# Kernel optimization log

Hardware: AMD Instinct MI355X
Metric: run time of the kernel (lower is better)

The kernel has to match this reference:

```python
import jax, jax.numpy as jnp
import numpy as np

B, T, D = 4, 2048, 1024

def setup_inputs() -> dict:
    key = jax.random.key(0)
    kx, kq, kk, kv = jax.random.split(key, 4)
    return {
        "vector": jax.random.normal(kx, (B, T, D), dtype=jnp.float32),
        # original uses torch.rand -> uniform [0,1)
        "W_queries": jax.random.uniform(kq, (D, D), dtype=jnp.float32),
        "W_keys": jax.random.uniform(kk, (D, D), dtype=jnp.float32),
        "W_values": jax.random.uniform(kv, (D, D), dtype=jnp.float32),
    }

def reference(vector, W_queries, W_keys, W_values):
    b, num_token, d_out = vector.shape
    queries = vector @ W_queries          # [b, t, d]
    keys = vector @ W_keys                # [b, t, d]
    values = vector @ W_values            # [b, t, d]
    # attention_score: [b, q, k]
    scores = jnp.einsum('bqd,bkd->bqk', queries, keys)
    causal_mask = jnp.triu(jnp.ones((num_token, num_token), dtype=bool), k=1)
    scores = jnp.where(causal_mask[None, :, :], -jnp.inf, scores)
    # NOTE: original uses FLOOR division `//` by sqrt(d_k) -- faithful here.
    inv_sqrt_scale = jnp.asarray(np.sqrt(keys.shape[-1]), dtype=scores.dtype)
    weights = jnp.floor(scores / inv_sqrt_scale)
    # NOTE: original applies softmax over dim=1 (the query axis), not dim=-1.
    weights = jax.nn.softmax(weights, axis=1)
    # dropout rate is 0.0 (eval/deterministic): identity
    context = jnp.einsum('bqk,bkd->bqd', weights, values)
    return context
```

## Files before the change

kernel.cpp:

```cpp
#include <hip/hip_runtime.h>
#include <math.h>

typedef _Float16 half4 __attribute__((ext_vector_type(4)));
typedef _Float16 half8 __attribute__((ext_vector_type(8)));
typedef float f32x4 __attribute__((ext_vector_type(4)));

#define GLD16(gptr, lptr)                                                     \
    __builtin_amdgcn_global_load_lds(                                         \
        (const __attribute__((address_space(1))) unsigned int*)(gptr),        \
        (__attribute__((address_space(3))) unsigned int*)(lptr), 16, 0, 0)

#define PIPE_SYNC()                                                           \
    do {                                                                      \
        asm volatile("s_waitcnt vmcnt(0)" ::: "memory");                      \
        __builtin_amdgcn_s_barrier();                                         \
    } while (0)

namespace {

constexpr int Bb = 4;
constexpr int Tt = 2048;
constexpr int Dd = 1024;
constexpr int BT = Bb * Tt;
constexpr int NCH = 16;

__device__ inline _Float16 f2h(float f) { return (_Float16)f; }

__global__ __launch_bounds__(256) void convert_x_kernel(
    const float* __restrict__ X, _Float16* __restrict__ Xhi, _Float16* __restrict__ Xlo)
{
    const int idx = (blockIdx.x * 256 + threadIdx.x) * 4;
    const float4 v = *(const float4*)(X + idx);
    const float a[4] = {v.x, v.y, v.z, v.w};
    half4 h, l;
#pragma unroll
    for (int i = 0; i < 4; ++i) {
        h[i] = f2h(a[i]);
        l[i] = f2h(a[i] - (float)h[i]);
    }
    *(half4*)(Xhi + idx) = h;
    *(half4*)(Xlo + idx) = l;
}

__global__ __launch_bounds__(256) void convert_wqk_kernel(
    const float* __restrict__ Wq, const float* __restrict__ Wk,
    _Float16* __restrict__ Wqh, _Float16* __restrict__ Wql,
    _Float16* __restrict__ Wkh, _Float16* __restrict__ Wkl)
{
    const int mat = blockIdx.y;
    const float* W = mat ? Wk : Wq;
    _Float16* Hh = mat ? Wkh : Wqh;
    _Float16* Ll = mat ? Wkl : Wql;
    const int idx = (blockIdx.x * 256 + threadIdx.x) * 4;
    const float4 v = *(const float4*)(W + idx);
    const float a[4] = {v.x, v.y, v.z, v.w};
    half4 h, l;
#pragma unroll
    for (int i = 0; i < 4; ++i) {
        h[i] = f2h(a[i]);
        l[i] = f2h(a[i] - (float)h[i]);
    }
    *(half4*)(Hh + idx) = h;
    *(half4*)(Ll + idx) = l;
}

__global__ __launch_bounds__(256) void convert_wv_kernel(
    const float* __restrict__ Wv, _Float16* __restrict__ WvTh)
{
    __shared__ float tile[64][65];
    const int n0 = blockIdx.x * 64, k0 = blockIdx.y * 64;
    const int tx = threadIdx.x & 63, ty = threadIdx.x >> 6;
#pragma unroll
    for (int i = 0; i < 16; ++i)
        tile[ty + i * 4][tx] = Wv[(size_t)(k0 + ty + i * 4) * Dd + n0 + tx];
    __syncthreads();
#pragma unroll
    for (int i = 0; i < 16; ++i) {
        const float v = tile[tx][ty + i * 4];
        WvTh[(size_t)(n0 + ty + i * 4) * Dd + k0 + tx] = f2h(v);
    }
}

__global__ __launch_bounds__(256) void gt_kernel(
    const _Float16* __restrict__ Wkh, const _Float16* __restrict__ Wkl,
    const _Float16* __restrict__ Wqh, const _Float16* __restrict__ Wql,
    _Float16* __restrict__ GTh, _Float16* __restrict__ GTl)
{
    __shared__ _Float16 Ahl[2][2][4][512];
    __shared__ _Float16 Bhl[2][2][4][512];

    const int n0 = blockIdx.x * 64;
    const int m0 = blockIdx.y * 64;
    const int tid = threadIdx.x;
    const int w = tid >> 6, lane = tid & 63;
    const int lr = lane & 15, lq = lane >> 4;
    const int wi = (w >> 1) * 2, wj = (w & 1) * 2;

    f32x4 acc[2][2];
#pragma unroll
    for (int i = 0; i < 2; ++i)
#pragma unroll
        for (int j = 0; j < 2; ++j)
#pragma unroll
            for (int c = 0; c < 4; ++c) acc[i][j][c] = 0.f;

    auto stage = [&](int bf, int kk) {
        const int s = w;
        const size_t ar = (size_t)(m0 + s * 16 + lr) * Dd + kk + lq * 8;
        const size_t br = (size_t)(n0 + s * 16 + lr) * Dd + kk + lq * 8;
        GLD16(Wkh + ar, &Ahl[bf][0][s][0]);
        GLD16(Wkl + ar, &Ahl[bf][1][s][0]);
        GLD16(Wqh + br, &Bhl[bf][0][s][0]);
        GLD16(Wql + br, &Bhl[bf][1][s][0]);
    };

    stage(0, 0);
    PIPE_SYNC();
    int ib = 0;
    for (int kk = 0; kk < 1024; kk += 32, ib ^= 1) {
        if (kk + 32 < 1024) stage(ib ^ 1, kk + 32);
        half8 ah[2], al[2], bh[2], bl[2];
#pragma unroll
        for (int i = 0; i < 2; ++i) {
            ah[i] = *(const half8*)&Ahl[ib][0][wi + i][lane * 8];
            al[i] = *(const half8*)&Ahl[ib][1][wi + i][lane * 8];
        }
#pragma unroll
        for (int j = 0; j < 2; ++j) {
            bh[j] = *(const half8*)&Bhl[ib][0][wj + j][lane * 8];
            bl[j] = *(const half8*)&Bhl[ib][1][wj + j][lane * 8];
        }
#pragma unroll
        for (int i = 0; i < 2; ++i)
#pragma unroll
            for (int j = 0; j < 2; ++j) {
                acc[i][j] = __builtin_amdgcn_mfma_f32_16x16x32_f16(ah[i], bh[j], acc[i][j], 0, 0, 0);
                acc[i][j] = __builtin_amdgcn_mfma_f32_16x16x32_f16(ah[i], bl[j], acc[i][j], 0, 0, 0);
                acc[i][j] = __builtin_amdgcn_mfma_f32_16x16x32_f16(al[i], bh[j], acc[i][j], 0, 0, 0);
            }
        PIPE_SYNC();
    }

#pragma unroll
    for (int i = 0; i < 2; ++i)
#pragma unroll
        for (int r = 0; r < 4; ++r) {
            const int row = m0 + (wi + i) * 16 + lq * 4 + r;
#pragma unroll
            for (int j = 0; j < 2; ++j) {
                const int col = n0 + (wj + j) * 16 + lr;
                const float v = acc[i][j][r];
                const _Float16 h = f2h(v);
                GTh[(size_t)row * Dd + col] = h;
                GTl[(size_t)row * Dd + col] = f2h(v - (float)h);
            }
        }
}

__global__ __launch_bounds__(256, 4) void tv_kernel(
    const _Float16* __restrict__ Xhi, const _Float16* __restrict__ Xlo,
    const _Float16* __restrict__ GTh, const _Float16* __restrict__ GTl,
    const _Float16* __restrict__ WvTh,
    _Float16* __restrict__ Thi, _Float16* __restrict__ Tlo,
    _Float16* __restrict__ Vrow)
{
    __shared__ _Float16 Ahl[2][8][512];
    __shared__ _Float16 Bhl[2][8][512];

    const int f  = blockIdx.x;
    const int fp = (f & 7) * 128 + (f >> 3);
    const int mb  = fp >> 4;
    const int sub = fp & 15;
    const int m0 = mb * 128;
    const int n0 = (sub & 7) * 128;

    const int tid = threadIdx.x;
    const int w = tid >> 6, lane = tid & 63;
    const int lr = lane & 15, lq = lane >> 4;
    const int wr = (w >> 1) * 4, wc = (w & 1) * 4;

    f32x4 acc[4][4];
#pragma unroll
    for (int i = 0; i < 4; ++i)
#pragma unroll
        for (int j = 0; j < 4; ++j)
#pragma unroll
            for (int c = 0; c < 4; ++c) acc[i][j][c] = 0.f;

    if (sub < 8) {
        for (int kk = 0; kk < 1024; kk += 32) {
            __syncthreads();
#pragma unroll
            for (int s2 = 0; s2 < 2; ++s2) {
                const int s = w * 2 + s2;
                const size_t ar = (size_t)(m0 + s * 16 + lr) * Dd + kk + lq * 8;
                const size_t br = (size_t)(n0 + s * 16 + lr) * Dd + kk + lq * 8;
                GLD16(Xhi + ar, &Ahl[0][s][0]);
                GLD16(Xlo + ar, &Ahl[1][s][0]);
                GLD16(GTh + br, &Bhl[0][s][0]);
                GLD16(GTl + br, &Bhl[1][s][0]);
            }
            __syncthreads();
            half8 ah[4], al[4], bh[4], bl[4];
#pragma unroll
            for (int i = 0; i < 4; ++i) {
                ah[i] = *(const half8*)&Ahl[0][wr + i][lane * 8];
                al[i] = *(const half8*)&Ahl[1][wr + i][lane * 8];
            }
#pragma unroll
            for (int j = 0; j < 4; ++j) {
                bh[j] = *(const half8*)&Bhl[0][wc + j][lane * 8];
                bl[j] = *(const half8*)&Bhl[1][wc + j][lane * 8];
            }
#pragma unroll
            for (int i = 0; i < 4; ++i)
#pragma unroll
                for (int j = 0; j < 4; ++j) {
                    acc[i][j] = __builtin_amdgcn_mfma_f32_16x16x32_f16(ah[i], bh[j], acc[i][j], 0, 0, 0);
                    acc[i][j] = __builtin_amdgcn_mfma_f32_16x16x32_f16(ah[i], bl[j], acc[i][j], 0, 0, 0);
                    acc[i][j] = __builtin_amdgcn_mfma_f32_16x16x32_f16(al[i], bh[j], acc[i][j], 0, 0, 0);
                }
        }
#pragma unroll
        for (int i = 0; i < 4; ++i)
#pragma unroll
            for (int r = 0; r < 4; ++r) {
                const int row = m0 + (wr + i) * 16 + lq * 4 + r;
#pragma unroll
                for (int j = 0; j < 4; ++j) {
                    const int col = n0 + (wc + j) * 16 + lr;
                    const float v = acc[i][j][r];
                    const _Float16 h = f2h(v);
                    Thi[(size_t)row * Dd + col] = h;
                    Tlo[(size_t)row * Dd + col] = f2h(v - (float)h);
                }
            }
    } else {
        for (int kk = 0; kk < 1024; kk += 32) {
            __syncthreads();
#pragma unroll
            for (int s2 = 0; s2 < 2; ++s2) {
                const int s = w * 2 + s2;
                GLD16(Xhi + (size_t)(m0 + s * 16 + lr) * Dd + kk + lq * 8, &Ahl[0][s][0]);
                GLD16(WvTh + (size_t)(n0 + s * 16 + lr) * Dd + kk + lq * 8, &Bhl[0][s][0]);
            }
            __syncthreads();
            half8 a[4], b2[4];
#pragma unroll
            for (int i = 0; i < 4; ++i) a[i] = *(const half8*)&Ahl[0][wr + i][lane * 8];
#pragma unroll
            for (int j = 0; j < 4; ++j) b2[j] = *(const half8*)&Bhl[0][wc + j][lane * 8];
#pragma unroll
            for (int i = 0; i < 4; ++i)
#pragma unroll
                for (int j = 0; j < 4; ++j)
                    acc[i][j] = __builtin_amdgcn_mfma_f32_16x16x32_f16(a[i], b2[j], acc[i][j], 0, 0, 0);
        }
#pragma unroll
        for (int i = 0; i < 4; ++i)
#pragma unroll
            for (int r = 0; r < 4; ++r) {
                const int row = m0 + (wr + i) * 16 + lq * 4 + r;
#pragma unroll
                for (int j = 0; j < 4; ++j)
                    Vrow[(size_t)row * Dd + n0 + (wc + j) * 16 + lr] = f2h(acc[i][j][r]);
            }
    }
}

__global__ __launch_bounds__(256) void transpose_v_kernel(
    const _Float16* __restrict__ Vrow, const float* __restrict__ Lb,
    _Float16* __restrict__ Vt)
{
    __shared__ _Float16 tile[64][78];
    const int d0 = blockIdx.x * 64, t0 = blockIdx.y * 64, b = blockIdx.z;
    const int tx = threadIdx.x & 63, ty = threadIdx.x >> 6;
#pragma unroll
    for (int i = 0; i < 16; ++i)
        tile[ty + i * 4][tx] = Vrow[((size_t)b * Tt + t0 + ty + i * 4) * Dd + d0 + tx];
    __syncthreads();
    const float sc = Lb[(size_t)b * Tt + t0 + tx];
#pragma unroll
    for (int i = 0; i < 16; ++i) {
        const float v = (float)tile[tx][ty + i * 4] * sc;
        Vt[(size_t)b * Dd * Tt + (size_t)(d0 + ty + i * 4) * Tt + t0 + tx] = f2h(v);
    }
}

__global__ __launch_bounds__(256) void scores_mfma_kernel(
    const _Float16* __restrict__ Thi, const _Float16* __restrict__ Tlo,
    const _Float16* __restrict__ Xhi, const _Float16* __restrict__ Xlo,
    float* __restrict__ S, float* __restrict__ Pm, float* __restrict__ Pl)
{
    const int f  = blockIdx.x;
    const int fp = (f & 7) * 68 + (f >> 3);
    const int b = fp / 136;
    const int t = fp - b * 136;
    int byi = (int)((sqrtf(8.f * t + 1.f) - 1.f) * 0.5f);
    if ((byi + 1) * (byi + 2) / 2 <= t) ++byi;
    if (byi * (byi + 1) / 2 > t) --byi;
    const int bxi = t - byi * (byi + 1) / 2;
    const int j0 = bxi * 128, q0 = byi * 128;
    float* Sb = S + (size_t)b * Tt * Tt;

    __shared__ _Float16 Ahl[2][2][8][512];
    __shared__ _Float16 Bhl[2][2][8][512];
    const _Float16* Th = Thi + (size_t)b * Tt * Dd;
    const _Float16* Tl = Tlo + (size_t)b * Tt * Dd;
    const _Float16* Xh = Xhi + (size_t)b * Tt * Dd;
    const _Float16* Xl = Xlo + (size_t)b * Tt * Dd;

    const int tid = threadIdx.x;
    const int w = tid >> 6, lane = tid & 63;
    const int lr = lane & 15, lq = lane >> 4;
    const int wr = (w >> 1) * 4, wc = (w & 1) * 4;

    f32x4 acc[4][4];
#pragma unroll
    for (int i = 0; i < 4; ++i)
#pragma unroll
        for (int j = 0; j < 4; ++j)
#pragma unroll
            for (int c = 0; c < 4; ++c) acc[i][j][c] = 0.f;

    auto stage = [&](int bf, int kk) {
#pragma unroll
        for (int s2 = 0; s2 < 2; ++s2) {
            const int s = w * 2 + s2;
            const size_t ar = (size_t)(q0 + s * 16 + lr) * Dd + kk + lq * 8;
            const size_t br = (size_t)(j0 + s * 16 + lr) * Dd + kk + lq * 8;
            GLD16(Th + ar, &Ahl[bf][0][s][0]);
            GLD16(Tl + ar, &Ahl[bf][1][s][0]);
            GLD16(Xh + br, &Bhl[bf][0][s][0]);
            GLD16(Xl + br, &Bhl[bf][1][s][0]);
        }
    };

    stage(0, 0);
    PIPE_SYNC();
    int ib = 0;
    for (int kk = 0; kk < 1024; kk += 32, ib ^= 1) {
        if (kk + 32 < 1024) stage(ib ^ 1, kk + 32);
        half8 ah[4], al[4], bh[4], bl[4];
#pragma unroll
        for (int i = 0; i < 4; ++i) {
            ah[i] = *(const half8*)&Ahl[ib][0][wr + i][lane * 8];
            al[i] = *(const half8*)&Ahl[ib][1][wr + i][lane * 8];
        }
#pragma unroll
        for (int j = 0; j < 4; ++j) {
            bh[j] = *(const half8*)&Bhl[ib][0][wc + j][lane * 8];
            bl[j] = *(const half8*)&Bhl[ib][1][wc + j][lane * 8];
        }
#pragma unroll
        for (int i = 0; i < 4; ++i)
#pragma unroll
            for (int j = 0; j < 4; ++j) {
                acc[i][j] = __builtin_amdgcn_mfma_f32_16x16x32_f16(ah[i], bh[j], acc[i][j], 0, 0, 0);
                acc[i][j] = __builtin_amdgcn_mfma_f32_16x16x32_f16(ah[i], bl[j], acc[i][j], 0, 0, 0);
                acc[i][j] = __builtin_amdgcn_mfma_f32_16x16x32_f16(al[i], bh[j], acc[i][j], 0, 0, 0);
            }
        PIPE_SYNC();
    }

    float sv[4][4][4];
#pragma unroll
    for (int i = 0; i < 4; ++i)
#pragma unroll
        for (int r = 0; r < 4; ++r) {
            const int q = q0 + (wr + i) * 16 + lq * 4 + r;
#pragma unroll
            for (int j = 0; j < 4; ++j) {
                const int jg = j0 + (wc + j) * 16 + lr;
                const float v = (jg <= q) ? floorf(acc[i][j][r] * 0.03125f) : -INFINITY;
                sv[i][j][r] = v;
                Sb[(size_t)q * Tt + jg] = v;
            }
        }

    float* red  = (float*)&Ahl[0][0][0][0];
    float* colm = red + 2048;
    __syncthreads();
    for (int e = tid; e < 2048; e += 256) red[e] = -INFINITY;
    __syncthreads();
    const int rowidx = (w * 4 + lq) * 128;
#pragma unroll
    for (int j = 0; j < 4; ++j) {
        const int c = (wc + j) * 16 + lr;
        float lm = -INFINITY;
#pragma unroll
        for (int i = 0; i < 4; ++i)
#pragma unroll
            for (int r = 0; r < 4; ++r) lm = fmaxf(lm, sv[i][j][r]);
        red[rowidx + c] = lm;
    }
    __syncthreads();
    if (tid < 128) {
        float m = -INFINITY;
#pragma unroll
        for (int e = 0; e < 16; ++e) m = fmaxf(m, red[e * 128 + tid]);
        colm[tid] = m;
    }
    __syncthreads();
    float ls[4];
#pragma unroll
    for (int j = 0; j < 4; ++j) {
        const int c = (wc + j) * 16 + lr;
        const float m = colm[c];
        float s = 0.f;
#pragma unroll
        for (int i = 0; i < 4; ++i)
#pragma unroll
            for (int r = 0; r < 4; ++r)
                if (sv[i][j][r] != -INFINITY) s += __expf(sv[i][j][r] - m);
        ls[j] = s;
    }
    __syncthreads();
    for (int e = tid; e < 2048; e += 256) red[e] = 0.f;
    __syncthreads();
#pragma unroll
    for (int j = 0; j < 4; ++j) red[rowidx + (wc + j) * 16 + lr] = ls[j];
    __syncthreads();
    if (tid < 128) {
        float l = 0.f;
#pragma unroll
        for (int e = 0; e < 16; ++e) l += red[e * 128 + tid];
        const size_t o = ((size_t)b * NCH + byi) * Tt + j0 + tid;
        Pm[o] = colm[tid];
        Pl[o] = l;
    }
}

__global__ __launch_bounds__(256) void colstats_merge_kernel(
    const float* __restrict__ Pm, const float* __restrict__ Pl,
    float* __restrict__ Mb, float* __restrict__ Lb)
{
    const int j = blockIdx.x * 256 + threadIdx.x;
    const int b = blockIdx.y;
    const int jt = j >> 7;
    float m = -INFINITY, l = 0.f;
    for (int c = jt; c < NCH; ++c) {
        const size_t pidx = ((size_t)b * NCH + c) * Tt + j;
        const float mi = Pm[pidx];
        if (mi == -INFINITY) continue;
        const float li = Pl[pidx];
        if (mi > m) { l = l * __expf(m - mi) + li; m = mi; }
        else        { l += li * __expf(mi - m); }
    }
    Mb[(size_t)b * Tt + j] = m;
    Lb[(size_t)b * Tt + j] = (l > 0.f) ? 1.f / l : 0.f;
}

__global__ __launch_bounds__(256) void pmat_kernel(
    const float* __restrict__ S, const float* __restrict__ Mb,
    _Float16* __restrict__ P)
{
    const int t = blockIdx.x;
    int byi = (int)((sqrtf(8.f * t + 1.f) - 1.f) * 0.5f);
    if ((byi + 1) * (byi + 2) / 2 <= t) ++byi;
    if (byi * (byi + 1) / 2 > t) --byi;
    const int bxi = t - byi * (byi + 1) / 2;
    const int b = blockIdx.z;
    const int j0 = bxi * 128, q0 = byi * 128;

    const int tr = threadIdx.x >> 4;
    const int tc = (threadIdx.x & 15) * 8;
    const float* mp = Mb + (size_t)b * Tt + j0 + tc;
    float mv[8];
#pragma unroll
    for (int e = 0; e < 8; ++e) mv[e] = mp[e];

#pragma unroll
    for (int it = 0; it < 8; ++it) {
        const int row = q0 + it * 16 + tr;
        const float* Sp = S + (size_t)b * Tt * Tt + (size_t)row * Tt + j0 + tc;
        const float4 s0 = *(const float4*)Sp;
        const float4 s1 = *(const float4*)(Sp + 4);
        const float sa[8] = {s0.x, s0.y, s0.z, s0.w, s1.x, s1.y, s1.z, s1.w};
        half8 out;
#pragma unroll
        for (int e = 0; e < 8; ++e) {
            const int jg = j0 + tc + e;
            out[e] = (jg <= row) ? f2h(__expf(sa[e] - mv[e])) : (_Float16)0.f;
        }
        *(half8*)(P + (size_t)b * Tt * Tt + (size_t)row * Tt + j0 + tc) = out;
    }
}

__global__ __launch_bounds__(256) void context_mfma_kernel(
    const _Float16* __restrict__ P, const _Float16* __restrict__ Vt,
    float* __restrict__ Out)
{
    __shared__ _Float16 Al[2][8][512];
    __shared__ _Float16 Bl[2][8][512];

    const int f  = blockIdx.x;
    const int fp = (f & 7) * 64 + (f >> 3);
    const int b  = fp >> 7;
    const int r  = fp & 127;
    const int bx = r & 7;
    const int tq = r >> 3;
    const int by = (tq & 1) ? (15 - (tq >> 1)) : (tq >> 1);
    const int d0 = bx * 128;
    const int q0 = by * 128;
    const _Float16* Pb = P + (size_t)b * Tt * Tt;
    const _Float16* Vb = Vt + (size_t)b * Dd * Tt;
    float* Ob = Out + (size_t)b * Tt * Dd;

    const int tid = threadIdx.x;
    const int w = tid >> 6, lane = tid & 63;
    const int lr = lane & 15, lq = lane >> 4;
    const int wr = (w >> 1) * 4, wc = (w & 1) * 4;

    f32x4 acc[4][4];
#pragma unroll
    for (int i = 0; i < 4; ++i)
#pragma unroll
        for (int j = 0; j < 4; ++j)
#pragma unroll
            for (int c = 0; c < 4; ++c) acc[i][j][c] = 0.f;

    auto stage = [&](int bf, int k0) {
#pragma unroll
        for (int s2 = 0; s2 < 2; ++s2) {
            const int s = w * 2 + s2;
            GLD16(Pb + (size_t)(q0 + s * 16 + lr) * Tt + k0 + lq * 8, &Al[bf][s][0]);
            GLD16(Vb + (size_t)(d0 + s * 16 + lr) * Tt + k0 + lq * 8, &Bl[bf][s][0]);
        }
    };

    const int kmax = q0 + 128;
    stage(0, 0);
    PIPE_SYNC();
    int ib = 0;
    for (int k0 = 0; k0 < kmax; k0 += 32, ib ^= 1) {
        if (k0 + 32 < kmax) stage(ib ^ 1, k0 + 32);
        half8 a[4], b2[4];
#pragma unroll
        for (int i = 0; i < 4; ++i) a[i] = *(const half8*)&Al[ib][wr + i][lane * 8];
#pragma unroll
        for (int j = 0; j < 4; ++j) b2[j] = *(const half8*)&Bl[ib][wc + j][lane * 8];
#pragma unroll
        for (int i = 0; i < 4; ++i)
#pragma unroll
            for (int j = 0; j < 4; ++j)
                acc[i][j] = __builtin_amdgcn_mfma_f32_16x16x32_f16(a[i], b2[j], acc[i][j], 0, 0, 0);
        PIPE_SYNC();
    }

#pragma unroll
    for (int i = 0; i < 4; ++i)
#pragma unroll
        for (int r2 = 0; r2 < 4; ++r2) {
            const int row = q0 + (wr + i) * 16 + lq * 4 + r2;
#pragma unroll
            for (int j = 0; j < 4; ++j)
                Ob[(size_t)row * Dd + d0 + (wc + j) * 16 + lr] = acc[i][j][r2];
        }
}

}

extern "C" void kernel_launch(void* const* d_in, const int* in_sizes, int n_in,
                              void* d_out, int out_size, void* d_ws, size_t ws_size,
                              hipStream_t stream)
{
    const float* X  = (const float*)d_in[0];
    const float* Wq = (const float*)d_in[1];
    const float* Wk = (const float*)d_in[2];
    const float* Wv = (const float*)d_in[3];

    char* ws = (char*)d_ws;
    const size_t MB = 1024 * 1024;
    _Float16* Xhi  = (_Float16*)ws;
    _Float16* Xlo  = (_Float16*)(ws + 16 * MB);
    _Float16* Wqh  = (_Float16*)(ws + 32 * MB);
    _Float16* Wql  = (_Float16*)(ws + 34 * MB);
    _Float16* Wkh  = (_Float16*)(ws + 36 * MB);
    _Float16* Wkl  = (_Float16*)(ws + 38 * MB);
    _Float16* WvTh = (_Float16*)(ws + 40 * MB);
    _Float16* GTh  = (_Float16*)(ws + 44 * MB);
    _Float16* GTl  = (_Float16*)(ws + 46 * MB);
    _Float16* Thi  = (_Float16*)(ws + 48 * MB);
    _Float16* Tlo  = (_Float16*)(ws + 64 * MB);
    _Float16* P    = Thi;
    _Float16* Vt   = (_Float16*)(ws + 80 * MB);
    _Float16* Vrow = (_Float16*)(ws + 96 * MB);
    float*    S    = (float*)(ws + 112 * MB);
    float*    Mb   = (float*)(ws + 176 * MB);
    float*    Lb   = Mb + (size_t)Bb * Tt;
    float*    Pm   = Lb + (size_t)Bb * Tt;
    float*    Pl   = Pm + (size_t)Bb * NCH * Tt;
    float*    Out  = (float*)d_out;

    convert_x_kernel<<<BT * Dd / 1024, 256, 0, stream>>>(X, Xhi, Xlo);
    convert_wqk_kernel<<<dim3(Dd * Dd / 1024, 2), 256, 0, stream>>>(Wq, Wk, Wqh, Wql, Wkh, Wkl);
    convert_wv_kernel<<<dim3(16, 16), 256, 0, stream>>>(Wv, WvTh);
    gt_kernel<<<dim3(16, 16), 256, 0, stream>>>(Wkh, Wkl, Wqh, Wql, GTh, GTl);
    tv_kernel<<<dim3(1024), 256, 0, stream>>>(Xhi, Xlo, GTh, GTl, WvTh, Thi, Tlo, Vrow);
    scores_mfma_kernel<<<dim3(544), 256, 0, stream>>>(Thi, Tlo, Xhi, Xlo, S, Pm, Pl);
    colstats_merge_kernel<<<dim3(Tt / 256, Bb), 256, 0, stream>>>(Pm, Pl, Mb, Lb);
    transpose_v_kernel<<<dim3(Dd / 64, Tt / 64, Bb), 256, 0, stream>>>(Vrow, Lb, Vt);
    pmat_kernel<<<dim3(136, 1, Bb), 256, 0, stream>>>(S, Mb, P);
    context_mfma_kernel<<<dim3(512), 256, 0, stream>>>(P, Vt, Out);
}
```

Before: 457.2 us.

## Overlap next-tile global-to-LDS loads with MFMA via partial vmcnt waits

Each GEMM loop now issues the next tile's global_load_lds and then waits only for the previous tile's loads with a partial vmcnt count, rather than draining all loads before computing. This lets the prefetch overlap the MFMA work. The tv_kernel moves from a single-buffered loop with two __syncthreads per step to a double-buffered prefetch pipeline, which doubles its LDS footprint, so its launch bounds drop from 4 to 2 blocks per CU. Scheduling fences and explicit barriers are added, and the vmcnt counts must match the exact number of loads issued per stage or the results will be wrong.

New measurement: 452.0 us. No clear change (-1.1%).

```diff
diff --git a/kernel.cpp b/kernel.cpp
--- a/kernel.cpp
+++ b/kernel.cpp
@@ -10,11 +10,9 @@
         (const __attribute__((address_space(1))) unsigned int*)(gptr),        \
         (__attribute__((address_space(3))) unsigned int*)(lptr), 16, 0, 0)
 
-#define PIPE_SYNC()                                                           \
-    do {                                                                      \
-        asm volatile("s_waitcnt vmcnt(0)" ::: "memory");                      \
-        __builtin_amdgcn_s_barrier();                                         \
-    } while (0)
+#define WAIT_VM(N) asm volatile("s_waitcnt vmcnt(" #N ")" ::: "memory")
+#define BARRIER()  __builtin_amdgcn_s_barrier()
+#define SCHED_FENCE() __builtin_amdgcn_sched_barrier(0)
 
 namespace {
 
@@ -115,10 +113,16 @@
     };
 
     stage(0, 0);
-    PIPE_SYNC();
     int ib = 0;
-    for (int kk = 0; kk < 1024; kk += 32, ib ^= 1) {
-        if (kk + 32 < 1024) stage(ib ^ 1, kk + 32);
+    for (int step = 0; step < 32; ++step, ib ^= 1) {
+        if (step < 31) {
+            stage(ib ^ 1, (step + 1) << 5);
+            WAIT_VM(4);
+        } else {
+            WAIT_VM(0);
+        }
+        BARRIER();
+        SCHED_FENCE();
         half8 ah[2], al[2], bh[2], bl[2];
 #pragma unroll
         for (int i = 0; i < 2; ++i) {
@@ -138,7 +142,7 @@
                 acc[i][j] = __builtin_amdgcn_mfma_f32_16x16x32_f16(ah[i], bl[j], acc[i][j], 0, 0, 0);
                 acc[i][j] = __builtin_amdgcn_mfma_f32_16x16x32_f16(al[i], bh[j], acc[i][j], 0, 0, 0);
             }
-        PIPE_SYNC();
+        BARRIER();
     }
 
 #pragma unroll
@@ -157,15 +161,15 @@
         }
 }
 
-__global__ __launch_bounds__(256, 4) void tv_kernel(
+__global__ __launch_bounds__(256, 2) void tv_kernel(
     const _Float16* __restrict__ Xhi, const _Float16* __restrict__ Xlo,
     const _Float16* __restrict__ GTh, const _Float16* __restrict__ GTl,
     const _Float16* __restrict__ WvTh,
     _Float16* __restrict__ Thi, _Float16* __restrict__ Tlo,
     _Float16* __restrict__ Vrow)
 {
-    __shared__ _Float16 Ahl[2][8][512];
-    __shared__ _Float16 Bhl[2][8][512];
+    __shared__ _Float16 Ahl[2][2][8][512];
+    __shared__ _Float16 Bhl[2][2][8][512];
 
     const int f  = blockIdx.x;
     const int fp = (f & 7) * 128 + (f >> 3);
@@ -188,29 +192,39 @@
             for (int c = 0; c < 4; ++c) acc[i][j][c] = 0.f;
 
     if (sub < 8) {
-        for (int kk = 0; kk < 1024; kk += 32) {
-            __syncthreads();
+        auto stage = [&](int bf, int kk) {
 #pragma unroll
             for (int s2 = 0; s2 < 2; ++s2) {
                 const int s = w * 2 + s2;
                 const size_t ar = (size_t)(m0 + s * 16 + lr) * Dd + kk + lq * 8;
                 const size_t br = (size_t)(n0 + s * 16 + lr) * Dd + kk + lq * 8;
-                GLD16(Xhi + ar, &Ahl[0][s][0]);
-                GLD16(Xlo + ar, &Ahl[1][s][0]);
-                GLD16(GTh + br, &Bhl[0][s][0]);
-                GLD16(GTl + br, &Bhl[1][s][0]);
-            }
-            __syncthreads();
+                GLD16(Xhi + ar, &Ahl[bf][0][s][0]);
+                GLD16(Xlo + ar, &Ahl[bf][1][s][0]);
+                GLD16(GTh + br, &Bhl[bf][0][s][0]);
+                GLD16(GTl + br, &Bhl[bf][1][s][0]);
+            }
+        };
+        stage(0, 0);
+        int ib = 0;
+        for (int step = 0; step < 32; ++step, ib ^= 1) {
+            if (step < 31) {
+                stage(ib ^ 1, (step + 1) << 5);
+                WAIT_VM(8);
+            } else {
+                WAIT_VM(0);
+            }
+            BARRIER();
+            SCHED_FENCE();
             half8 ah[4], al[4], bh[4], bl[4];
 #pragma unroll
             for (int i = 0; i < 4; ++i) {
-                ah[i] = *(const half8*)&Ahl[0][wr + i][lane * 8];
-                al[i] = *(const half8*)&Ahl[1][wr + i][lane * 8];
+                ah[i] = *(const half8*)&Ahl[ib][0][wr + i][lane * 8];
+                al[i] = *(const half8*)&Ahl[ib][1][wr + i][lane * 8];
             }
 #pragma unroll
             for (int j = 0; j < 4; ++j) {
-                bh[j] = *(const half8*)&Bhl[0][wc + j][lane * 8];
-                bl[j] = *(const half8*)&Bhl[1][wc + j][lane * 8];
+                bh[j] = *(const half8*)&Bhl[ib][0][wc + j][lane * 8];
+                bl[j] = *(const half8*)&Bhl[ib][1][wc + j][lane * 8];
             }
 #pragma unroll
             for (int i = 0; i < 4; ++i)
@@ -220,6 +234,7 @@
                     acc[i][j] = __builtin_amdgcn_mfma_f32_16x16x32_f16(ah[i], bl[j], acc[i][j], 0, 0, 0);
                     acc[i][j] = __builtin_amdgcn_mfma_f32_16x16x32_f16(al[i], bh[j], acc[i][j], 0, 0, 0);
                 }
+            BARRIER();
         }
 #pragma unroll
         for (int i = 0; i < 4; ++i)
@@ -236,25 +251,36 @@
                 }
             }
     } else {
-        for (int kk = 0; kk < 1024; kk += 32) {
-            __syncthreads();
+        auto stage = [&](int bf, int kk) {
 #pragma unroll
             for (int s2 = 0; s2 < 2; ++s2) {
                 const int s = w * 2 + s2;
-                GLD16(Xhi + (size_t)(m0 + s * 16 + lr) * Dd + kk + lq * 8, &Ahl[0][s][0]);
-                GLD16(WvTh + (size_t)(n0 + s * 16 + lr) * Dd + kk + lq * 8, &Bhl[0][s][0]);
-            }
-            __syncthreads();
+                GLD16(Xhi + (size_t)(m0 + s * 16 + lr) * Dd + kk + lq * 8, &Ahl[bf][0][s][0]);
+                GLD16(WvTh + (size_t)(n0 + s * 16 + lr) * Dd + kk + lq * 8, &Bhl[bf][0][s][0]);
+            }
+        };
+        stage(0, 0);
+        int ib = 0;
+        for (int step = 0; step < 32; ++step, ib ^= 1) {
+            if (step < 31) {
+                stage(ib ^ 1, (step + 1) << 5);
+                WAIT_VM(4);
+            } else {
+                WAIT_VM(0);
+            }
+            BARRIER();
+            SCHED_FENCE();
             half8 a[4], b2[4];
 #pragma unroll
-            for (int i = 0; i < 4; ++i) a[i] = *(const half8*)&Ahl[0][wr + i][lane * 8];
-#pragma unroll
-            for (int j = 0; j < 4; ++j) b2[j] = *(const half8*)&Bhl[0][wc + j][lane * 8];
+            for (int i = 0; i < 4; ++i) a[i] = *(const half8*)&Ahl[ib][0][wr + i][lane * 8];
+#pragma unroll
+            for (int j = 0; j < 4; ++j) b2[j] = *(const half8*)&Bhl[ib][0][wc + j][lane * 8];
 #pragma unroll
             for (int i = 0; i < 4; ++i)
 #pragma unroll
                 for (int j = 0; j < 4; ++j)
                     acc[i][j] = __builtin_amdgcn_mfma_f32_16x16x32_f16(a[i], b2[j], acc[i][j], 0, 0, 0);
+            BARRIER();
         }
 #pragma unroll
         for (int i = 0; i < 4; ++i)
@@ -287,7 +313,7 @@
     }
 }
 
-__global__ __launch_bounds__(256) void scores_mfma_kernel(
+__global__ __launch_bounds__(256, 2) void scores_mfma_kernel(
     const _Float16* __restrict__ Thi, const _Float16* __restrict__ Tlo,
     const _Float16* __restrict__ Xhi, const _Float16* __restrict__ Xlo,
     float* __restrict__ S, float* __restrict__ Pm, float* __restrict__ Pl)
@@ -337,10 +363,16 @@
     };
 
     stage(0, 0);
-    PIPE_SYNC();
     int ib = 0;
-    for (int kk = 0; kk < 1024; kk += 32, ib ^= 1) {
-        if (kk + 32 < 1024) stage(ib ^ 1, kk + 32);
+    for (int step = 0; step < 32; ++step, ib ^= 1) {
+        if (step < 31) {
+            stage(ib ^ 1, (step + 1) << 5);
+            WAIT_VM(8);
+        } else {
+            WAIT_VM(0);
+        }
+        BARRIER();
+        SCHED_FENCE();
         half8 ah[4], al[4], bh[4], bl[4];
 #pragma unroll
         for (int i = 0; i < 4; ++i) {
@@ -360,7 +392,7 @@
                 acc[i][j] = __builtin_amdgcn_mfma_f32_16x16x32_f16(ah[i], bl[j], acc[i][j], 0, 0, 0);
                 acc[i][j] = __builtin_amdgcn_mfma_f32_16x16x32_f16(al[i], bh[j], acc[i][j], 0, 0, 0);
             }
-        PIPE_SYNC();
+        BARRIER();
     }
 
     float sv[4][4][4];
@@ -529,12 +561,18 @@
         }
     };
 
-    const int kmax = q0 + 128;
+    const int nstep = (q0 + 128) >> 5;
     stage(0, 0);
-    PIPE_SYNC();
     int ib = 0;
-    for (int k0 = 0; k0 < kmax; k0 += 32, ib ^= 1) {
-        if (k0 + 32 < kmax) stage(ib ^ 1, k0 + 32);
+    for (int step = 0; step < nstep; ++step, ib ^= 1) {
+        if (step + 1 < nstep) {
+            stage(ib ^ 1, (step + 1) << 5);
+            WAIT_VM(4);
+        } else {
+            WAIT_VM(0);
+        }
+        BARRIER();
+        SCHED_FENCE();
         half8 a[4], b2[4];
 #pragma unroll
         for (int i = 0; i < 4; ++i) a[i] = *(const half8*)&Al[ib][wr + i][lane * 8];
@@ -545,7 +583,7 @@
 #pragma unroll
             for (int j = 0; j < 4; ++j)
                 acc[i][j] = __builtin_amdgcn_mfma_f32_16x16x32_f16(a[i], b2[j], acc[i][j], 0, 0, 0);
-        PIPE_SYNC();
+        BARRIER();
     }
 
 #pragma unroll
```

## Replace LDS-staged GEMM operand loads with direct global-to-register double buffering

Applied to the files above, without the earlier changes.

All MFMA GEMM kernels (gt, tv, scores, context) stop staging operand tiles through shared memory with global_load_lds and barriers. Each wave now loads its fragments straight from global memory into registers, using two register sets ping-ponged over 32-wide k steps. This removes LDS traffic and block barriers, but each wave refetches operands that other waves share, which raises global/L2 traffic and register pressure. The launch-bounds occupancy hint on tv_kernel is also dropped.

Result: slower. 660.1 us (+44.4%).

```diff
diff --git a/kernel.cpp b/kernel.cpp
--- a/kernel.cpp
+++ b/kernel.cpp
@@ -4,17 +4,6 @@
 typedef _Float16 half4 __attribute__((ext_vector_type(4)));
 typedef _Float16 half8 __attribute__((ext_vector_type(8)));
 typedef float f32x4 __attribute__((ext_vector_type(4)));
-
-#define GLD16(gptr, lptr)                                                     \
-    __builtin_amdgcn_global_load_lds(                                         \
-        (const __attribute__((address_space(1))) unsigned int*)(gptr),        \
-        (__attribute__((address_space(3))) unsigned int*)(lptr), 16, 0, 0)
-
-#define PIPE_SYNC()                                                           \
-    do {                                                                      \
-        asm volatile("s_waitcnt vmcnt(0)" ::: "memory");                      \
-        __builtin_amdgcn_s_barrier();                                         \
-    } while (0)
 
 namespace {
 
@@ -86,15 +75,19 @@
     const _Float16* __restrict__ Wqh, const _Float16* __restrict__ Wql,
     _Float16* __restrict__ GTh, _Float16* __restrict__ GTl)
 {
-    __shared__ _Float16 Ahl[2][2][4][512];
-    __shared__ _Float16 Bhl[2][2][4][512];
-
     const int n0 = blockIdx.x * 64;
     const int m0 = blockIdx.y * 64;
     const int tid = threadIdx.x;
     const int w = tid >> 6, lane = tid & 63;
     const int lr = lane & 15, lq = lane >> 4;
     const int wi = (w >> 1) * 2, wj = (w & 1) * 2;
+    const int koff = lq * 8;
+
+    int aoff[2], boff[2];
+#pragma unroll
+    for (int i = 0; i < 2; ++i) aoff[i] = (m0 + (wi + i) * 16 + lr) * Dd + koff;
+#pragma unroll
+    for (int j = 0; j < 2; ++j) boff[j] = (n0 + (wj + j) * 16 + lr) * Dd + koff;
 
     f32x4 acc[2][2];
 #pragma unroll
@@ -104,32 +97,22 @@
 #pragma unroll
             for (int c = 0; c < 4; ++c) acc[i][j][c] = 0.f;
 
-    auto stage = [&](int bf, int kk) {
-        const int s = w;
-        const size_t ar = (size_t)(m0 + s * 16 + lr) * Dd + kk + lq * 8;
-        const size_t br = (size_t)(n0 + s * 16 + lr) * Dd + kk + lq * 8;
-        GLD16(Wkh + ar, &Ahl[bf][0][s][0]);
-        GLD16(Wkl + ar, &Ahl[bf][1][s][0]);
-        GLD16(Wqh + br, &Bhl[bf][0][s][0]);
-        GLD16(Wql + br, &Bhl[bf][1][s][0]);
+    half8 pah[2], pal[2], pbh[2], pbl[2];
+    half8 qah[2], qal[2], qbh[2], qbl[2];
+
+    auto load = [&](half8 (&ah)[2], half8 (&al)[2], half8 (&bh)[2], half8 (&bl)[2], int k) {
+#pragma unroll
+        for (int i = 0; i < 2; ++i) {
+            ah[i] = *(const half8*)(Wkh + aoff[i] + k);
+            al[i] = *(const half8*)(Wkl + aoff[i] + k);
+        }
+#pragma unroll
+        for (int j = 0; j < 2; ++j) {
+            bh[j] = *(const half8*)(Wqh + boff[j] + k);
+            bl[j] = *(const half8*)(Wql + boff[j] + k);
+        }
     };
-
-    stage(0, 0);
-    PIPE_SYNC();
-    int ib = 0;
-    for (int kk = 0; kk < 1024; kk += 32, ib ^= 1) {
-        if (kk + 32 < 1024) stage(ib ^ 1, kk + 32);
-        half8 ah[2], al[2], bh[2], bl[2];
-#pragma unroll
-        for (int i = 0; i < 2; ++i) {
-            ah[i] = *(const half8*)&Ahl[ib][0][wi + i][lane * 8];
-            al[i] = *(const half8*)&Ahl[ib][1][wi + i][lane * 8];
-        }
-#pragma unroll
-        for (int j = 0; j < 2; ++j) {
-            bh[j] = *(const half8*)&Bhl[ib][0][wj + j][lane * 8];
-            bl[j] = *(const half8*)&Bhl[ib][1][wj + j][lane * 8];
-        }
+    auto mf = [&](half8 (&ah)[2], half8 (&al)[2], half8 (&bh)[2], half8 (&bl)[2]) {
 #pragma unroll
         for (int i = 0; i < 2; ++i)
 #pragma unroll
@@ -138,7 +121,14 @@
                 acc[i][j] = __builtin_amdgcn_mfma_f32_16x16x32_f16(ah[i], bl[j], acc[i][j], 0, 0, 0);
                 acc[i][j] = __builtin_amdgcn_mfma_f32_16x16x32_f16(al[i], bh[j], acc[i][j], 0, 0, 0);
             }
-        PIPE_SYNC();
+    };
+
+    load(pah, pal, pbh, pbl, 0);
+    for (int kk = 0; kk < 1024; kk += 64) {
+        load(qah, qal, qbh, qbl, kk + 32);
+        mf(pah, pal, pbh, pbl);
+        if (kk + 64 < 1024) load(pah, pal, pbh, pbl, kk + 64);
+        mf(qah, qal, qbh, qbl);
     }
 
 #pragma unroll
@@ -157,16 +147,13 @@
         }
 }
 
-__global__ __launch_bounds__(256, 4) void tv_kernel(
+__global__ __launch_bounds__(256) void tv_kernel(
     const _Float16* __restrict__ Xhi, const _Float16* __restrict__ Xlo,
     const _Float16* __restrict__ GTh, const _Float16* __restrict__ GTl,
     const _Float16* __restrict__ WvTh,
     _Float16* __restrict__ Thi, _Float16* __restrict__ Tlo,
     _Float16* __restrict__ Vrow)
 {
-    __shared__ _Float16 Ahl[2][8][512];
-    __shared__ _Float16 Bhl[2][8][512];
-
     const int f  = blockIdx.x;
     const int fp = (f & 7) * 128 + (f >> 3);
     const int mb  = fp >> 4;
@@ -178,6 +165,13 @@
     const int w = tid >> 6, lane = tid & 63;
     const int lr = lane & 15, lq = lane >> 4;
     const int wr = (w >> 1) * 4, wc = (w & 1) * 4;
+    const int koff = lq * 8;
+
+    int aoff[4], boff[4];
+#pragma unroll
+    for (int i = 0; i < 4; ++i) aoff[i] = (m0 + (wr + i) * 16 + lr) * Dd + koff;
+#pragma unroll
+    for (int j = 0; j < 4; ++j) boff[j] = (n0 + (wc + j) * 16 + lr) * Dd + koff;
 
     f32x4 acc[4][4];
 #pragma unroll
@@ -188,30 +182,21 @@
             for (int c = 0; c < 4; ++c) acc[i][j][c] = 0.f;
 
     if (sub < 8) {
-        for (int kk = 0; kk < 1024; kk += 32) {
-            __syncthreads();
-#pragma unroll
-            for (int s2 = 0; s2 < 2; ++s2) {
-                const int s = w * 2 + s2;
-                const size_t ar = (size_t)(m0 + s * 16 + lr) * Dd + kk + lq * 8;
-                const size_t br = (size_t)(n0 + s * 16 + lr) * Dd + kk + lq * 8;
-                GLD16(Xhi + ar, &Ahl[0][s][0]);
-                GLD16(Xlo + ar, &Ahl[1][s][0]);
-                GLD16(GTh + br, &Bhl[0][s][0]);
-                GLD16(GTl + br, &Bhl[1][s][0]);
-            }
-            __syncthreads();
-            half8 ah[4], al[4], bh[4], bl[4];
+        half8 pah[4], pal[4], pbh[4], pbl[4];
+        half8 qah[4], qal[4], qbh[4], qbl[4];
+        auto load = [&](half8 (&ah)[4], half8 (&al)[4], half8 (&bh)[4], half8 (&bl)[4], int k) {
 #pragma unroll
             for (int i = 0; i < 4; ++i) {
-                ah[i] = *(const half8*)&Ahl[0][wr + i][lane * 8];
-                al[i] = *(const half8*)&Ahl[1][wr + i][lane * 8];
+                ah[i] = *(const half8*)(Xhi + aoff[i] + k);
+                al[i] = *(const half8*)(Xlo + aoff[i] + k);
             }
 #pragma unroll
             for (int j = 0; j < 4; ++j) {
-                bh[j] = *(const half8*)&Bhl[0][wc + j][lane * 8];
-                bl[j] = *(const half8*)&Bhl[1][wc + j][lane * 8];
-            }
+                bh[j] = *(const half8*)(GTh + boff[j] + k);
+                bl[j] = *(const half8*)(GTl + boff[j] + k);
+            }
+        };
+        auto mf = [&](half8 (&ah)[4], half8 (&al)[4], half8 (&bh)[4], half8 (&bl)[4]) {
 #pragma unroll
             for (int i = 0; i < 4; ++i)
 #pragma unroll
@@ -220,6 +205,13 @@
                     acc[i][j] = __builtin_amdgcn_mfma_f32_16x16x32_f16(ah[i], bl[j], acc[i][j], 0, 0, 0);
                     acc[i][j] = __builtin_amdgcn_mfma_f32_16x16x32_f16(al[i], bh[j], acc[i][j], 0, 0, 0);
                 }
+        };
+        load(pah, pal, pbh, pbl, 0);
+        for (int kk = 0; kk < 1024; kk += 64) {
+            load(qah, qal, qbh, qbl, kk + 32);
+            mf(pah, pal, pbh, pbl);
+            if (kk + 64 < 1024) load(pah, pal, pbh, pbl, kk + 64);
+            mf(qah, qal, qbh, qbl);
         }
 #pragma unroll
         for (int i = 0; i < 4; ++i)
@@ -236,25 +228,26 @@
                 }
             }
     } else {
-        for (int kk = 0; kk < 1024; kk += 32) {
-            __syncthreads();
-#pragma unroll
-            for (int s2 = 0; s2 < 2; ++s2) {
-                const int s = w * 2 + s2;
-                GLD16(Xhi + (size_t)(m0 + s * 16 + lr) * Dd + kk + lq * 8, &Ahl[0][s][0]);
-                GLD16(WvTh + (size_t)(n0 + s * 16 + lr) * Dd + kk + lq * 8, &Bhl[0][s][0]);
-            }
-            __syncthreads();
-            half8 a[4], b2[4];
-#pragma unroll
-            for (int i = 0; i < 4; ++i) a[i] = *(const half8*)&Ahl[0][wr + i][lane * 8];
-#pragma unroll
-            for (int j = 0; j < 4; ++j) b2[j] = *(const half8*)&Bhl[0][wc + j][lane * 8];
+        half8 pa[4], pb[4], qa[4], qb[4];
+        auto load = [&](half8 (&a)[4], half8 (&b)[4], int k) {
+#pragma unroll
+            for (int i = 0; i < 4; ++i) a[i] = *(const half8*)(Xhi + aoff[i] + k);
+#pragma unroll
+            for (int j = 0; j < 4; ++j) b[j] = *(const half8*)(WvTh + boff[j] + k);
+        };
+        auto mf = [&](half8 (&a)[4], half8 (&b)[4]) {
 #pragma unroll
             for (int i = 0; i < 4; ++i)
 #pragma unroll
                 for (int j = 0; j < 4; ++j)
-                    acc[i][j] = __builtin_amdgcn_mfma_f32_16x16x32_f16(a[i], b2[j], acc[i][j], 0, 0, 0);
+                    acc[i][j] = __builtin_amdgcn_mfma_f32_16x16x32_f16(a[i], b[j], acc[i][j], 0, 0, 0);
+        };
+        load(pa, pb, 0);
+        for (int kk = 0; kk < 1024; kk += 64) {
+            load(qa, qb, kk + 32);
+            mf(pa, pb);
+            if (kk + 64 < 1024) load(pa, pb, kk + 64);
+            mf(qa, qb);
         }
 #pragma unroll
         for (int i = 0; i < 4; ++i)
@@ -292,6 +285,9 @@
     const _Float16* __restrict__ Xhi, const _Float16* __restrict__ Xlo,
     float* __restrict__ S, float* __restrict__ Pm, float* __restrict__ Pl)
 {
+    __shared__ float red[2048];
+    __shared__ float colm[128];
+
     const int f  = blockIdx.x;
     const int fp = (f & 7) * 68 + (f >> 3);
     const int b = fp / 136;
@@ -303,8 +299,6 @@
     const int j0 = bxi * 128, q0 = byi * 128;
     float* Sb = S + (size_t)b * Tt * Tt;
 
-    __shared__ _Float16 Ahl[2][2][8][512];
-    __shared__ _Float16 Bhl[2][2][8][512];
     const _Float16* Th = Thi + (size_t)b * Tt * Dd;
     const _Float16* Tl = Tlo + (size_t)b * Tt * Dd;
     const _Float16* Xh = Xhi + (size_t)b * Tt * Dd;
@@ -314,6 +308,13 @@
     const int w = tid >> 6, lane = tid & 63;
     const int lr = lane & 15, lq = lane >> 4;
     const int wr = (w >> 1) * 4, wc = (w & 1) * 4;
+    const int koff = lq * 8;
+
+    int aoff[4], boff[4];
+#pragma unroll
+    for (int i = 0; i < 4; ++i) aoff[i] = (q0 + (wr + i) * 16 + lr) * Dd + koff;
+#pragma unroll
+    for (int j = 0; j < 4; ++j) boff[j] = (j0 + (wc + j) * 16 + lr) * Dd + koff;
 
     f32x4 acc[4][4];
 #pragma unroll
@@ -323,35 +324,21 @@
 #pragma unroll
             for (int c = 0; c < 4; ++c) acc[i][j][c] = 0.f;
 
-    auto stage = [&](int bf, int kk) {
-#pragma unroll
-        for (int s2 = 0; s2 < 2; ++s2) {
-            const int s = w * 2 + s2;
-            const size_t ar = (size_t)(q0 + s * 16 + lr) * Dd + kk + lq * 8;
-            const size_t br = (size_t)(j0 + s * 16 + lr) * Dd + kk + lq * 8;
-            GLD16(Th + ar, &Ahl[bf][0][s][0]);
-            GLD16(Tl + ar, &Ahl[bf][1][s][0]);
-            GLD16(Xh + br, &Bhl[bf][0][s][0]);
-            GLD16(Xl + br, &Bhl[bf][1][s][0]);
+    half8 pah[4], pal[4], pbh[4], pbl[4];
+    half8 qah[4], qal[4], qbh[4], qbl[4];
+    auto load = [&](half8 (&ah)[4], half8 (&al)[4], half8 (&bh)[4], half8 (&bl)[4], int k) {
+#pragma unroll
+        for (int i = 0; i < 4; ++i) {
+            ah[i] = *(const half8*)(Th + aoff[i] + k);
+            al[i] = *(const half8*)(Tl + aoff[i] + k);
+        }
+#pragma unroll
+        for (int j = 0; j < 4; ++j) {
+            bh[j] = *(const half8*)(Xh + boff[j] + k);
+            bl[j] = *(const half8*)(Xl + boff[j] + k);
         }
     };
-
-    stage(0, 0);
-    PIPE_SYNC();
-    int ib = 0;
-    for (int kk = 0; kk < 1024; kk += 32, ib ^= 1) {
-        if (kk + 32 < 1024) stage(ib ^ 1, kk + 32);
-        half8 ah[4], al[4], bh[4], bl[4];
-#pragma unroll
-        for (int i = 0; i < 4; ++i) {
-            ah[i] = *(const half8*)&Ahl[ib][0][wr + i][lane * 8];
-            al[i] = *(const half8*)&Ahl[ib][1][wr + i][lane * 8];
-        }
-#pragma unroll
-        for (int j = 0; j < 4; ++j) {
-            bh[j] = *(const half8*)&Bhl[ib][0][wc + j][lane * 8];
-            bl[j] = *(const half8*)&Bhl[ib][1][wc + j][lane * 8];
-        }
+    auto mf = [&](half8 (&ah)[4], half8 (&al)[4], half8 (&bh)[4], half8 (&bl)[4]) {
 #pragma unroll
         for (int i = 0; i < 4; ++i)
 #pragma unroll
@@ -360,7 +347,14 @@
                 acc[i][j] = __builtin_amdgcn_mfma_f32_16x16x32_f16(ah[i], bl[j], acc[i][j], 0, 0, 0);
                 acc[i][j] = __builtin_amdgcn_mfma_f32_16x16x32_f16(al[i], bh[j], acc[i][j], 0, 0, 0);
             }
-        PIPE_SYNC();
+    };
+
+    load(pah, pal, pbh, pbl, 0);
+    for (int kk = 0; kk < 1024; kk += 64) {
+        load(qah, qal, qbh, qbl, kk + 32);
+        mf(pah, pal, pbh, pbl);
+        if (kk + 64 < 1024) load(pah, pal, pbh, pbl, kk + 64);
+        mf(qah, qal, qbh, qbl);
     }
 
     float sv[4][4][4];
@@ -378,8 +372,6 @@
             }
         }
 
-    float* red  = (float*)&Ahl[0][0][0][0];
-    float* colm = red + 2048;
     __syncthreads();
     for (int e = tid; e < 2048; e += 256) red[e] = -INFINITY;
     __syncthreads();
@@ -491,9 +483,6 @@
     const _Float16* __restrict__ P, const _Float16* __restrict__ Vt,
     float* __restrict__ Out)
 {
-    __shared__ _Float16 Al[2][8][512];
-    __shared__ _Float16 Bl[2][8][512];
-
     const int f  = blockIdx.x;
     const int fp = (f & 7) * 64 + (f >> 3);
     const int b  = fp >> 7;
@@ -511,6 +500,13 @@
     const int w = tid >> 6, lane = tid & 63;
     const int lr = lane & 15, lq = lane >> 4;
     const int wr = (w >> 1) * 4, wc = (w & 1) * 4;
+    const int koff = lq * 8;
+
+    int aoff[4], boff[4];
+#pragma unroll
+    for (int i = 0; i < 4; ++i) aoff[i] = (q0 + (wr + i) * 16 + lr) * Tt + koff;
+#pragma unroll
+    for (int j = 0; j < 4; ++j) boff[j] = (d0 + (wc + j) * 16 + lr) * Tt + koff;
 
     f32x4 acc[4][4];
 #pragma unroll
@@ -520,32 +516,28 @@
 #pragma unroll
             for (int c = 0; c < 4; ++c) acc[i][j][c] = 0.f;
 
-    auto stage = [&](int bf, int k0) {
-#pragma unroll
-        for (int s2 = 0; s2 < 2; ++s2) {
-            const int s = w * 2 + s2;
-            GLD16(Pb + (size_t)(q0 + s * 16 + lr) * Tt + k0 + lq * 8, &Al[bf][s][0]);
-            GLD16(Vb + (size_t)(d0 + s * 16 + lr) * Tt + k0 + lq * 8, &Bl[bf][s][0]);
-        }
+    half8 pa[4], pb2[4], qa[4], qb2[4];
+    auto load = [&](half8 (&a)[4], half8 (&b2)[4], int k) {
+#pragma unroll
+        for (int i = 0; i < 4; ++i) a[i] = *(const half8*)(Pb + aoff[i] + k);
+#pragma unroll
+        for (int j = 0; j < 4; ++j) b2[j] = *(const half8*)(Vb + boff[j] + k);
     };
-
-    const int kmax = q0 + 128;
-    stage(0, 0);
-    PIPE_SYNC();
-    int ib = 0;
-    for (int k0 = 0; k0 < kmax; k0 += 32, ib ^= 1) {
-        if (k0 + 32 < kmax) stage(ib ^ 1, k0 + 32);
-        half8 a[4], b2[4];
-#pragma unroll
-        for (int i = 0; i < 4; ++i) a[i] = *(const half8*)&Al[ib][wr + i][lane * 8];
-#pragma unroll
-        for (int j = 0; j < 4; ++j) b2[j] = *(const half8*)&Bl[ib][wc + j][lane * 8];
+    auto mf = [&](half8 (&a)[4], half8 (&b2)[4]) {
 #pragma unroll
         for (int i = 0; i < 4; ++i)
 #pragma unroll
             for (int j = 0; j < 4; ++j)
                 acc[i][j] = __builtin_amdgcn_mfma_f32_16x16x32_f16(a[i], b2[j], acc[i][j], 0, 0, 0);
-        PIPE_SYNC();
+    };
+
+    const int kmax = q0 + 128;
+    load(pa, pb2, 0);
+    for (int kk = 0; kk < kmax; kk += 64) {
+        load(qa, qb2, kk + 32);
+        mf(pa, pb2);
+        if (kk + 64 < kmax) load(pa, pb2, kk + 64);
+        mf(qa, qb2);
     }
 
 #pragma unroll
```
